# Kernel optimization log

Measured on AMD Instinct MI355X. Metric: run time of the kernel, lower is better.

Reference implementation:

```python
import jax, jax.numpy as jnp
import numpy as np

NQ, DEPTH = 4, 2
C64 = jnp.complex64


def _ry(theta):
    # theta: scalar or (B,) -> (...,2,2) complex
    h = theta.astype(jnp.float32) / 2
    c, s = jnp.cos(h).astype(C64), jnp.sin(h).astype(C64)
    return jnp.stack([jnp.stack([c, -s], -1), jnp.stack([s, c], -1)], -2)


def _rot(phi, theta, omega):
    # PennyLane Rot = RZ(omega) @ RY(theta) @ RZ(phi), scalars -> (2,2) complex
    h = theta / 2
    c, s = jnp.cos(h), jnp.sin(h)
    ep = jnp.exp(-0.5j * (phi + omega).astype(C64))
    em = jnp.exp(0.5j * (phi - omega).astype(C64))
    return jnp.array(1.0, C64) * jnp.stack([
        jnp.stack([ep * c, -em * s], -1),
        jnp.stack([jnp.conj(em) * s, jnp.conj(ep) * c], -1)], -2)


def _apply_1q(state, U, wire):
    # state: (B,2,2,2,2); U: (2,2) or (B,2,2)
    s = jnp.moveaxis(state, wire + 1, -1)
    if U.ndim == 2:
        s = jnp.einsum('ij,bklmj->bklmi', U, s)
    else:
        s = jnp.einsum('bij,bklmj->bklmi', U, s)
    return jnp.moveaxis(s, -1, wire + 1)


def _cnot(state, ctrl, tgt):
    s = jnp.moveaxis(state, [ctrl + 1, tgt + 1], [-2, -1])
    s = s.at[..., 1, :].set(s[..., 1, ::-1])
    return jnp.moveaxis(s, [-2, -1], [ctrl + 1, tgt + 1])


def _circuit(x, q_weights):
    B = x.shape[0]
    state = jnp.zeros((B, 2, 2, 2, 2), C64).at[:, 0, 0, 0, 0].set(1.0)
    # angle encoding: RY(x[:, w]) on wire w (batched gates)
    for w in range(NQ):
        state = _apply_1q(state, _ry(x[:, w]), w)
    # variational layers
    for layer in range(DEPTH):
        for w in range(NQ):
            U = _rot(q_weights[layer, w, 0], q_weights[layer, w, 1], q_weights[layer, w, 2])
            state = _apply_1q(state, U, w)
        for w in range(NQ - 1):
            state = _cnot(state, w, w + 1)
        state = _cnot(state, NQ - 1, 0)  # num_qubits > 2 wrap-around
    # expval PauliZ on each wire
    probs = jnp.abs(state) ** 2  # (B,2,2,2,2) float32
    z = jnp.array([1.0, -1.0], jnp.float32)
    outs = [jnp.einsum('bijkl,' + 'ijkl'[w] + '->b', probs, z) for w in range(NQ)]
    return jnp.stack(outs, axis=1).astype(x.dtype)  # (B, 4)


def setup_inputs() -> dict:
    key = jax.random.key(0)
    k1, k2 = jax.random.split(key)
    B = 2_000_000
    x = jax.random.uniform(k1, (B, NQ), jnp.float32, minval=0.0, maxval=np.pi)
    q_weights = jax.random.normal(k2, (DEPTH, NQ, 3), jnp.float32) * 0.01
    return {"x": x, "q_weights": q_weights}


def reference(x, q_weights):
    return _circuit(x, q_weights)
```

## Files before the change

kernel.cpp:

```cpp
#include <hip/hip_runtime.h>

#define NQ 4
#define DEPTH 2
#define BLK 256
#define K 4

typedef _Float16 v2h __attribute__((ext_vector_type(2)));

__device__ __forceinline__ float fdot2u(unsigned u, unsigned p, float acc) {
#if __has_builtin(__builtin_amdgcn_fdot2)
    return __builtin_amdgcn_fdot2(__builtin_bit_cast(v2h, u),
                                  __builtin_bit_cast(v2h, p), acc, false);
#else
    float d;
    asm("v_dot2_f32_f16 %0, %1, %2, %3" : "=v"(d) : "v"(u), "v"(p), "v"(acc));
    return d;
#endif
}
__device__ __forceinline__ unsigned pack2h(float a, float b) {
    return __builtin_bit_cast(unsigned, __builtin_amdgcn_cvt_pkrtz(a, b));
}

__device__ __forceinline__ float2 cmul(float2 a, float2 b) {
    return make_float2(a.x * b.x - a.y * b.y, a.x * b.y + a.y * b.x);
}
__device__ __forceinline__ float2 cadd(float2 a, float2 b) {
    return make_float2(a.x + b.x, a.y + b.y);
}

__device__ __forceinline__ void build_u_col(const float* __restrict__ qw, int col,
                                            float2 amp[16]) {
#pragma unroll
    for (int i = 0; i < 16; i++)
        amp[i] = make_float2((i == col) ? 1.f : 0.f, 0.f);

#pragma unroll
    for (int layer = 0; layer < DEPTH; layer++) {
#pragma unroll
        for (int w = 0; w < NQ; w++) {
            const float* g = qw + (layer * NQ + w) * 3;
            float phi = g[0], theta = g[1], omega = g[2];
            float ch, sh, sp, cp, sm, cm;
            __sincosf(0.5f * theta, &sh, &ch);
            __sincosf(-0.5f * (phi + omega), &sp, &cp);
            __sincosf(0.5f * (phi - omega), &sm, &cm);
            float2 U00 = make_float2(cp * ch, sp * ch);
            float2 U01 = make_float2(-cm * sh, -sm * sh);
            float2 U10 = make_float2(cm * sh, -sm * sh);
            float2 U11 = make_float2(cp * ch, -sp * ch);
            const int mask = 8 >> w;
#pragma unroll
            for (int i0 = 0; i0 < 16; i0++) {
                if (i0 & mask) continue;
                const int i1 = i0 | mask;
                float2 a0 = amp[i0], a1 = amp[i1];
                amp[i0] = cadd(cmul(U00, a0), cmul(U01, a1));
                amp[i1] = cadd(cmul(U10, a0), cmul(U11, a1));
            }
        }
#pragma unroll
        for (int c = 0; c < NQ; c++) {
            const int t = (c + 1) & 3;
            const int cmsk = 8 >> c, tmsk = 8 >> t;
#pragma unroll
            for (int i = 0; i < 16; i++) {
                if ((i & cmsk) && !(i & tmsk)) {
                    float2 tmp = amp[i];
                    amp[i] = amp[i | tmsk];
                    amp[i | tmsk] = tmp;
                }
            }
        }
    }
}

__global__ void build_u_kernel(const float* __restrict__ qw, _Float16* __restrict__ Uw) {
    const int tid = threadIdx.x;
    if (tid < 16) {
        float2 amp[16];
        build_u_col(qw, tid, amp);
        _Float16* wre = Uw;
        _Float16* wim = Uw + 256;
#pragma unroll
        for (int i = 0; i < 16; i++) {
            wre[i * 16 + tid] = (_Float16)amp[i].x;
            wim[i * 16 + tid] = (_Float16)amp[i].y;
        }
    }
}

__device__ __forceinline__ void vqc_body(const float* __restrict__ x,
                                         const unsigned* Upl,
                                         float* __restrict__ out, int B) {
    const int tid = threadIdx.x;
    const int base = blockIdx.x * (BLK * K) + tid;

    bool val[K];
    unsigned psh[K][8];
#pragma unroll
    for (int k = 0; k < K; k++) {
        const int b = base + k * BLK;
        val[k] = (b < B);
        const float4 v = val[k] ? ((const float4*)x)[b] : make_float4(0.f, 0.f, 0.f, 0.f);
        const float R = 0.07957747154594767f;
        float s0 = __builtin_amdgcn_sinf(v.x * R), c0 = __builtin_amdgcn_cosf(v.x * R);
        float s1 = __builtin_amdgcn_sinf(v.y * R), c1 = __builtin_amdgcn_cosf(v.y * R);
        float s2 = __builtin_amdgcn_sinf(v.z * R), c2 = __builtin_amdgcn_cosf(v.z * R);
        float s3 = __builtin_amdgcn_sinf(v.w * R), c3 = __builtin_amdgcn_cosf(v.w * R);
        const float a01[4] = {c0 * c1, c0 * s1, s0 * c1, s0 * s1};
        const float a23[4] = {c2 * c3, c2 * s3, s2 * c3, s2 * s3};
#pragma unroll
        for (int q = 0; q < 8; q++) {
            const int j0 = 2 * q, j1 = 2 * q + 1;
            psh[k][q] = pack2h(a01[j0 >> 2] * a23[j0 & 3], a01[j1 >> 2] * a23[j1 & 3]);
        }
    }

    float ow0[K], ow1[K], ow2[K], ow3[K];
#pragma unroll
    for (int k = 0; k < K; k++) { ow0[k] = 0.f; ow1[k] = 0.f; ow2[k] = 0.f; ow3[k] = 0.f; }

#pragma unroll 1
    for (int rp = 0; rp < 8; rp++) {
        const int r0 = 2 * rp;
        const uint4 re0a = *(const uint4*)&Upl[r0 * 8];
        const uint4 re0b = *(const uint4*)&Upl[r0 * 8 + 4];
        const uint4 re1a = *(const uint4*)&Upl[(r0 + 1) * 8];
        const uint4 re1b = *(const uint4*)&Upl[(r0 + 1) * 8 + 4];
        const uint4 im0a = *(const uint4*)&Upl[128 + r0 * 8];
        const uint4 im0b = *(const uint4*)&Upl[128 + r0 * 8 + 4];
        const uint4 im1a = *(const uint4*)&Upl[128 + (r0 + 1) * 8];
        const uint4 im1b = *(const uint4*)&Upl[128 + (r0 + 1) * 8 + 4];
        const unsigned ur0[8] = {re0a.x, re0a.y, re0a.z, re0a.w, re0b.x, re0b.y, re0b.z, re0b.w};
        const unsigned ur1[8] = {re1a.x, re1a.y, re1a.z, re1a.w, re1b.x, re1b.y, re1b.z, re1b.w};
        const unsigned ui0[8] = {im0a.x, im0a.y, im0a.z, im0a.w, im0b.x, im0b.y, im0b.z, im0b.w};
        const unsigned ui1[8] = {im1a.x, im1a.y, im1a.z, im1a.w, im1b.x, im1b.y, im1b.z, im1b.w};

        const float f3 = (rp & 4) ? -1.f : 1.f;
        const float f2 = (rp & 2) ? -1.f : 1.f;
        const float f1 = (rp & 1) ? -1.f : 1.f;

#pragma unroll
        for (int k = 0; k < K; k++) {
            float fre0 = 0.f, fim0 = 0.f, fre1 = 0.f, fim1 = 0.f;
#pragma unroll
            for (int q = 0; q < 8; q++) {
                const unsigned p = psh[k][q];
                fre0 = fdot2u(ur0[q], p, fre0);
                fim0 = fdot2u(ui0[q], p, fim0);
                fre1 = fdot2u(ur1[q], p, fre1);
                fim1 = fdot2u(ui1[q], p, fim1);
            }
            const float p0 = fmaf(fim0, fim0, fre0 * fre0);
            const float p1 = fmaf(fim1, fim1, fre1 * fre1);
            const float s = p0 + p1, d = p0 - p1;
            ow0[k] = fmaf(f3, s, ow0[k]);
            ow1[k] = fmaf(f2, s, ow1[k]);
            ow2[k] = fmaf(f1, s, ow2[k]);
            ow3[k] += d;
        }
    }

#pragma unroll
    for (int k = 0; k < K; k++) {
        const int b = base + k * BLK;
        if (val[k])
            ((float4*)out)[b] = make_float4(ow0[k], ow1[k], ow2[k], ow3[k]);
    }
}

__global__ __launch_bounds__(BLK) void vqc_main(const float* __restrict__ x,
                                                const uint4* __restrict__ Uw,
                                                float* __restrict__ out, int B) {
    __shared__ __align__(16) unsigned Upl[256];
    if (threadIdx.x < 64) ((uint4*)Upl)[threadIdx.x] = Uw[threadIdx.x];
    __syncthreads();
    vqc_body(x, Upl, out, B);
}

__global__ void vqc_fused(const float* __restrict__ x, const float* __restrict__ qw,
                          float* __restrict__ out, int B) {
    __shared__ __align__(16) unsigned Upl[256];
    if (threadIdx.x < 16) {
        float2 amp[16];
        build_u_col(qw, threadIdx.x, amp);
        _Float16* wre = (_Float16*)Upl;
        _Float16* wim = wre + 256;
#pragma unroll
        for (int i = 0; i < 16; i++) {
            wre[i * 16 + threadIdx.x] = (_Float16)amp[i].x;
            wim[i * 16 + threadIdx.x] = (_Float16)amp[i].y;
        }
    }
    __syncthreads();
    vqc_body(x, Upl, out, B);
}

extern "C" void kernel_launch(void* const* d_in, const int* in_sizes, int n_in,
                              void* d_out, int out_size, void* d_ws, size_t ws_size,
                              hipStream_t stream) {
    const float* x  = (const float*)d_in[0];
    const float* qw = (const float*)d_in[1];
    float* out = (float*)d_out;
    const int B = in_sizes[0] / NQ;
    const int blocks = (B + BLK * K - 1) / (BLK * K);

    if (ws_size >= 1024) {
        build_u_kernel<<<1, 64, 0, stream>>>(qw, (_Float16*)d_ws);
        vqc_main<<<blocks, BLK, 0, stream>>>(x, (const uint4*)d_ws, out, B);
    } else {
        vqc_fused<<<blocks, BLK, 0, stream>>>(x, qw, out, B);
    }
}
```

Measured before the change: 105.8 us.

## Fuse unitary build into main kernel, prefetch inputs, double rows per thread

Drops the separate build_u kernel launch. Every block now builds the 16x16 fused circuit unitary in shared memory itself, and the x loads are issued before that build so their latency overlaps with the trig setup. Rows per thread go from 4 to 8, which halves the grid and spreads the per-block unitary build over more work. The cost is more registers per thread (8x8 packed amplitudes plus accumulators), which may lower occupancy, and every block repeats the unitary computation.

```diff
diff --git a/kernel.cpp b/kernel.cpp
--- a/kernel.cpp
+++ b/kernel.cpp
@@ -3,7 +3,7 @@
 #define NQ 4
 #define DEPTH 2
 #define BLK 256
-#define K 4
+#define K 8
 
 typedef _Float16 v2h __attribute__((ext_vector_type(2)));
 
@@ -74,39 +74,44 @@
     }
 }
 
-__global__ void build_u_kernel(const float* __restrict__ qw, _Float16* __restrict__ Uw) {
+__global__ __launch_bounds__(BLK) void vqc_fused(const float* __restrict__ x,
+                                                 const float* __restrict__ qw,
+                                                 float* __restrict__ out, int B) {
+    __shared__ __align__(16) unsigned Upl[256];
+
     const int tid = threadIdx.x;
+    const int base = blockIdx.x * (BLK * K) + tid;
+
+    bool val[K];
+    float4 v[K];
+#pragma unroll
+    for (int k = 0; k < K; k++) {
+        const int b = base + k * BLK;
+        val[k] = (b < B);
+        v[k] = val[k] ? ((const float4*)x)[b] : make_float4(0.f, 0.f, 0.f, 0.f);
+    }
+
     if (tid < 16) {
         float2 amp[16];
         build_u_col(qw, tid, amp);
-        _Float16* wre = Uw;
-        _Float16* wim = Uw + 256;
+        _Float16* wre = (_Float16*)Upl;
+        _Float16* wim = wre + 256;
 #pragma unroll
         for (int i = 0; i < 16; i++) {
             wre[i * 16 + tid] = (_Float16)amp[i].x;
             wim[i * 16 + tid] = (_Float16)amp[i].y;
         }
     }
-}
+    __syncthreads();
 
-__device__ __forceinline__ void vqc_body(const float* __restrict__ x,
-                                         const unsigned* Upl,
-                                         float* __restrict__ out, int B) {
-    const int tid = threadIdx.x;
-    const int base = blockIdx.x * (BLK * K) + tid;
-
-    bool val[K];
     unsigned psh[K][8];
 #pragma unroll
     for (int k = 0; k < K; k++) {
-        const int b = base + k * BLK;
-        val[k] = (b < B);
-        const float4 v = val[k] ? ((const float4*)x)[b] : make_float4(0.f, 0.f, 0.f, 0.f);
         const float R = 0.07957747154594767f;
-        float s0 = __builtin_amdgcn_sinf(v.x * R), c0 = __builtin_amdgcn_cosf(v.x * R);
-        float s1 = __builtin_amdgcn_sinf(v.y * R), c1 = __builtin_amdgcn_cosf(v.y * R);
-        float s2 = __builtin_amdgcn_sinf(v.z * R), c2 = __builtin_amdgcn_cosf(v.z * R);
-        float s3 = __builtin_amdgcn_sinf(v.w * R), c3 = __builtin_amdgcn_cosf(v.w * R);
+        float s0 = __builtin_amdgcn_sinf(v[k].x * R), c0 = __builtin_amdgcn_cosf(v[k].x * R);
+        float s1 = __builtin_amdgcn_sinf(v[k].y * R), c1 = __builtin_amdgcn_cosf(v[k].y * R);
+        float s2 = __builtin_amdgcn_sinf(v[k].z * R), c2 = __builtin_amdgcn_cosf(v[k].z * R);
+        float s3 = __builtin_amdgcn_sinf(v[k].w * R), c3 = __builtin_amdgcn_cosf(v[k].w * R);
         const float a01[4] = {c0 * c1, c0 * s1, s0 * c1, s0 * s1};
         const float a23[4] = {c2 * c3, c2 * s3, s2 * c3, s2 * s3};
 #pragma unroll
@@ -169,33 +174,6 @@
     }
 }
 
-__global__ __launch_bounds__(BLK) void vqc_main(const float* __restrict__ x,
-                                                const uint4* __restrict__ Uw,
-                                                float* __restrict__ out, int B) {
-    __shared__ __align__(16) unsigned Upl[256];
-    if (threadIdx.x < 64) ((uint4*)Upl)[threadIdx.x] = Uw[threadIdx.x];
-    __syncthreads();
-    vqc_body(x, Upl, out, B);
-}
-
-__global__ void vqc_fused(const float* __restrict__ x, const float* __restrict__ qw,
-                          float* __restrict__ out, int B) {
-    __shared__ __align__(16) unsigned Upl[256];
-    if (threadIdx.x < 16) {
-        float2 amp[16];
-        build_u_col(qw, threadIdx.x, amp);
-        _Float16* wre = (_Float16*)Upl;
-        _Float16* wim = wre + 256;
-#pragma unroll
-        for (int i = 0; i < 16; i++) {
-            wre[i * 16 + threadIdx.x] = (_Float16)amp[i].x;
-            wim[i * 16 + threadIdx.x] = (_Float16)amp[i].y;
-        }
-    }
-    __syncthreads();
-    vqc_body(x, Upl, out, B);
-}
-
 extern "C" void kernel_launch(void* const* d_in, const int* in_sizes, int n_in,
                               void* d_out, int out_size, void* d_ws, size_t ws_size,
                               hipStream_t stream) {
@@ -205,10 +183,5 @@
     const int B = in_sizes[0] / NQ;
     const int blocks = (B + BLK * K - 1) / (BLK * K);
 
-    if (ws_size >= 1024) {
-        build_u_kernel<<<1, 64, 0, stream>>>(qw, (_Float16*)d_ws);
-        vqc_main<<<blocks, BLK, 0, stream>>>(x, (const uint4*)d_ws, out, B);
-    } else {
-        vqc_fused<<<blocks, BLK, 0, stream>>>(x, qw, out, B);
-    }
+    vqc_fused<<<blocks, BLK, 0, stream>>>(x, qw, out, B);
 }
```

After: 107.6 us. No clear change (+1.7%).
